# Optimization experiments

Hardware: AMD Instinct MI355X
Metric: run time of the kernel (lower is better)

Reference implementation:

```python
import jax, jax.numpy as jnp
import numpy as np

EPS = 1e-6
G, S, N, K, O = 3, 10, 5000, 20, 1000  # groups, subjects, particles, communities, otus


def setup_inputs() -> dict:
    key = jax.random.key(0)
    k1, k2, k3, k4, k5 = jax.random.split(key, 5)
    # particle count data (nonnegative reads per OTU)
    counts = jax.random.uniform(k1, (G, S, N, O), dtype=jnp.float32) * 10.0
    # community OTU distributions (rows on simplex)
    otu_dist = jax.nn.softmax(jax.random.normal(k2, (K, O), dtype=jnp.float32), axis=-1)
    # community assignment distribution per (group, subject), normalized over K
    comm_dist = jax.nn.softmax(jax.random.normal(k3, (K, G, S), dtype=jnp.float32), axis=0)
    # contamination weight per group in (0, 1)
    contam_weight = jax.nn.sigmoid(jax.random.normal(k4, (G,), dtype=jnp.float32)) * 0.1
    # contamination community OTU distribution per group
    contam_comm = jax.nn.softmax(jax.random.normal(k5, (G, O), dtype=jnp.float32), axis=-1)
    gamma = jnp.ones((), dtype=jnp.float32)
    return {
        'counts': counts,
        'otu_dist': otu_dist,
        'comm_dist': comm_dist,
        'contam_weight': contam_weight,
        'contam_comm': contam_comm,
        'gamma': gamma,
    }


def reference(counts, otu_dist, comm_dist, contam_weight, contam_comm, gamma):
    # contamination mixture per group: [G, K, O]
    cw = contam_weight[:, None, None]
    mix = otu_dist[None, :, :] * (1.0 - cw) + cw * contam_comm[:, None, :]
    log_mix = jnp.log(mix + EPS)
    # (counts[:, None, :] * log_mix[None]).sum(-1) over all (g, s) at once:
    # scores[g, s, n, k] = sum_o counts[g, s, n, o] * log_mix[g, k, o]
    scores = jnp.einsum('gsno,gko->gsnk', counts, log_mix)
    # + log(comm_dist[None, :, g, s]) broadcast over particles
    scores = scores + jnp.log(comm_dist + EPS).transpose(1, 2, 0)[:, :, None, :]
    # sparse_logsumexp over community axis (dim=1 in original per-subject matrix)
    x_star = jnp.max(scores, axis=-1, keepdims=True)
    lse = x_star[..., 0] + jnp.log(jnp.sum(jnp.exp(gamma * (scores - x_star)), axis=-1))
    return jnp.sum(lse)
```

## Files before the change

kernel.cpp:

```cpp
#include <hip/hip_runtime.h>


#define EPSF 1e-6f
constexpr int Gc = 3, Sc = 10, Nc = 5000, Kc = 20, Oc = 1000;
constexpr int ROWS_PER_G = Sc * Nc;
constexpr int GRAN_ROWS  = 8;
constexpr int GRANS_PER_G = ROWS_PER_G / GRAN_ROWS;
constexpr int LM_ELEMS = Kc * Oc;
constexpr int LM_ALLOC = LM_ELEMS + 32;

__device__ __forceinline__ float red32(float v) {
  v += __int_as_float(__builtin_amdgcn_update_dpp(0, __float_as_int(v), 0x111, 0xF, 0xF, true));
  v += __int_as_float(__builtin_amdgcn_update_dpp(0, __float_as_int(v), 0x112, 0xF, 0xF, true));
  v += __int_as_float(__builtin_amdgcn_update_dpp(0, __float_as_int(v), 0x114, 0xF, 0xF, true));
  v += __int_as_float(__builtin_amdgcn_update_dpp(0, __float_as_int(v), 0x118, 0xF, 0xF, true));
  v += __int_as_float(__builtin_amdgcn_update_dpp(0, __float_as_int(v), 0x142, 0xF, 0xF, true));
  return v;
}

__global__ __launch_bounds__(512, 2) void perturb_kernel(
    const float* __restrict__ counts, const float* __restrict__ otu,
    const float* __restrict__ comm,   const float* __restrict__ cw,
    const float* __restrict__ cc,     const float* __restrict__ gamma_p,
    float* __restrict__ out) {
  __shared__ float s_lm[LM_ALLOC];
  __shared__ float s_bias[Sc * Kc];

  const int tid  = threadIdx.x;
  const int bid  = blockIdx.x;
  const int g    = bid % Gc;
  const int bg   = bid / Gc;
  const int blocksg = (gridDim.x + (Gc - 1) - g) / Gc;

  const float cwg = cw[g];
  const float gam = gamma_p[0];

  for (int idx = tid; idx < LM_ALLOC; idx += blockDim.x) {
    float v = 0.f;
    if (idx < LM_ELEMS) {
      int o = idx % Oc;
      float mix = otu[idx] * (1.f - cwg) + cwg * cc[g * Oc + o];
      v = __logf(mix + EPSF);
    }
    s_lm[idx] = v;
  }
  for (int idx = tid; idx < Sc * Kc; idx += blockDim.x) {
    int s = idx / Kc, k = idx - s * Kc;
    s_bias[idx] = __logf(comm[(k * Gc + g) * Sc + s] + EPSF);
  }
  __syncthreads();

  const int wave = tid >> 6;
  const int lane = tid & 63;
  const int rl   = lane >> 5;
  const int osub = lane & 31;

  const int waveg  = bg * 8 + wave;
  const int nwaveg = blocksg * 8;

  float lsum = 0.f;

  for (int gr = waveg; gr < GRANS_PER_G; gr += nwaveg) {
    const int row0 = gr * GRAN_ROWS + rl * 4;
    const float* base = counts + (size_t)(g * ROWS_PER_G + row0) * Oc;

    float acc[4][Kc];
#pragma unroll
    for (int r = 0; r < 4; ++r)
#pragma unroll
      for (int k = 0; k < Kc; ++k) acc[r][k] = 0.f;

    for (int j = 0; j < 7; ++j) {
      const int ob = j * 128 + (osub << 2);
      float4 c0 = *(const float4*)(base + 0 * Oc + ob);
      float4 c1 = *(const float4*)(base + 1 * Oc + ob);
      float4 c2 = *(const float4*)(base + 2 * Oc + ob);
      float4 c3 = *(const float4*)(base + 3 * Oc + ob);
#pragma unroll
      for (int k = 0; k < Kc; ++k) {
        float4 L = *(const float4*)&s_lm[k * Oc + ob];
        acc[0][k] += c0.x * L.x + c0.y * L.y + c0.z * L.z + c0.w * L.w;
        acc[1][k] += c1.x * L.x + c1.y * L.y + c1.z * L.z + c1.w * L.w;
        acc[2][k] += c2.x * L.x + c2.y * L.y + c2.z * L.z + c2.w * L.w;
        acc[3][k] += c3.x * L.x + c3.y * L.y + c3.z * L.z + c3.w * L.w;
      }
    }
    {
      const int ob = 896 + (osub << 2);
      float4 c0 = {0,0,0,0}, c1 = {0,0,0,0}, c2 = {0,0,0,0}, c3 = {0,0,0,0};
      if (osub < 26) {
        c0 = *(const float4*)(base + 0 * Oc + ob);
        c1 = *(const float4*)(base + 1 * Oc + ob);
        c2 = *(const float4*)(base + 2 * Oc + ob);
        c3 = *(const float4*)(base + 3 * Oc + ob);
      }
#pragma unroll
      for (int k = 0; k < Kc; ++k) {
        float4 L = *(const float4*)&s_lm[k * Oc + ob];
        acc[0][k] += c0.x * L.x + c0.y * L.y + c0.z * L.z + c0.w * L.w;
        acc[1][k] += c1.x * L.x + c1.y * L.y + c1.z * L.z + c1.w * L.w;
        acc[2][k] += c2.x * L.x + c2.y * L.y + c2.z * L.z + c2.w * L.w;
        acc[3][k] += c3.x * L.x + c3.y * L.y + c3.z * L.z + c3.w * L.w;
      }
    }

#pragma unroll
    for (int r = 0; r < 4; ++r)
#pragma unroll
      for (int k = 0; k < Kc; ++k) acc[r][k] = red32(acc[r][k]);

    if ((lane & 31) == 31) {
#pragma unroll
      for (int r = 0; r < 4; ++r) {
        const int s = (row0 + r) / Nc;
        const float* bp = &s_bias[s * Kc];
        float m = -3.4e38f;
#pragma unroll
        for (int k = 0; k < Kc; ++k) {
          float x = acc[r][k] + bp[k];
          acc[r][k] = x;
          m = fmaxf(m, x);
        }
        float sum = 0.f;
#pragma unroll
        for (int k = 0; k < Kc; ++k) sum += __expf(gam * (acc[r][k] - m));
        lsum += m + __logf(sum);
      }
    }
  }

  if ((lane & 31) == 31) atomicAdd(out, lsum);
}

extern "C" void kernel_launch(void* const* d_in, const int* in_sizes, int n_in,
                              void* d_out, int out_size, void* d_ws, size_t ws_size,
                              hipStream_t stream) {
  const float* counts = (const float*)d_in[0];
  const float* otu    = (const float*)d_in[1];
  const float* comm   = (const float*)d_in[2];
  const float* cw     = (const float*)d_in[3];
  const float* cc     = (const float*)d_in[4];
  const float* gam    = (const float*)d_in[5];
  float* out = (float*)d_out;

  hipMemsetAsync(out, 0, sizeof(float), stream);
  hipLaunchKernelGGL(perturb_kernel, dim3(512), dim3(512), 0, stream,
                     counts, otu, comm, cw, cc, gam, out);
}
```

Before: 884.9 us.

## Split communities across half-waves and software-prefetch count tiles into registers

Each wave now handles 4 rows, and its two half-waves each compute 10 of the 20 communities instead of each taking different rows. The two partial log-sum-exp results are merged with a cross-half shuffle. Count tiles for the next column chunk and the next granule are loaded into registers before the current chunk is used, to hide global-load latency. This halves the accumulator registers per lane and overlaps loads with FMAs, but both half-waves now load the same count data, doubling vector-memory instructions per row.

```diff
diff --git a/kernel.cpp b/kernel.cpp
--- a/kernel.cpp
+++ b/kernel.cpp
@@ -4,8 +4,9 @@
 #define EPSF 1e-6f
 constexpr int Gc = 3, Sc = 10, Nc = 5000, Kc = 20, Oc = 1000;
 constexpr int ROWS_PER_G = Sc * Nc;
-constexpr int GRAN_ROWS  = 8;
+constexpr int GRAN_ROWS  = 4;
 constexpr int GRANS_PER_G = ROWS_PER_G / GRAN_ROWS;
+constexpr int KH = Kc / 2;
 constexpr int LM_ELEMS = Kc * Oc;
 constexpr int LM_ALLOC = LM_ELEMS + 32;
 
@@ -52,84 +53,110 @@
 
   const int wave = tid >> 6;
   const int lane = tid & 63;
-  const int rl   = lane >> 5;
+  const int kh   = lane >> 5;
+  const int k0   = kh * KH;
   const int osub = lane & 31;
+  const int ocol = osub << 2;
 
   const int waveg  = bg * 8 + wave;
   const int nwaveg = blocksg * 8;
 
   float lsum = 0.f;
 
-  for (int gr = waveg; gr < GRANS_PER_G; gr += nwaveg) {
-    const int row0 = gr * GRAN_ROWS + rl * 4;
-    const float* base = counts + (size_t)(g * ROWS_PER_G + row0) * Oc;
+  int gr = waveg;
+  float4 cur0, cur1, cur2, cur3;
+  const float* gbase = counts + (size_t)g * ROWS_PER_G * Oc;
 
-    float acc[4][Kc];
+  if (gr < GRANS_PER_G) {
+    const float* base = gbase + (size_t)gr * GRAN_ROWS * Oc + ocol;
+    cur0 = *(const float4*)(base + 0 * Oc);
+    cur1 = *(const float4*)(base + 1 * Oc);
+    cur2 = *(const float4*)(base + 2 * Oc);
+    cur3 = *(const float4*)(base + 3 * Oc);
+  }
+
+  for (; gr < GRANS_PER_G; gr += nwaveg) {
+    const int row0 = gr * GRAN_ROWS;
+    const float* base = gbase + (size_t)row0 * Oc + ocol;
+
+    float acc[GRAN_ROWS][KH];
 #pragma unroll
-    for (int r = 0; r < 4; ++r)
+    for (int r = 0; r < GRAN_ROWS; ++r)
 #pragma unroll
-      for (int k = 0; k < Kc; ++k) acc[r][k] = 0.f;
+      for (int k = 0; k < KH; ++k) acc[r][k] = 0.f;
 
+#pragma unroll
     for (int j = 0; j < 7; ++j) {
-      const int ob = j * 128 + (osub << 2);
-      float4 c0 = *(const float4*)(base + 0 * Oc + ob);
-      float4 c1 = *(const float4*)(base + 1 * Oc + ob);
-      float4 c2 = *(const float4*)(base + 2 * Oc + ob);
-      float4 c3 = *(const float4*)(base + 3 * Oc + ob);
+      float4 n0 = {0,0,0,0}, n1 = {0,0,0,0}, n2 = {0,0,0,0}, n3 = {0,0,0,0};
+      if (j < 6 || osub < 26) {
+        const float* nb = base + (j + 1) * 128;
+        n0 = *(const float4*)(nb + 0 * Oc);
+        n1 = *(const float4*)(nb + 1 * Oc);
+        n2 = *(const float4*)(nb + 2 * Oc);
+        n3 = *(const float4*)(nb + 3 * Oc);
+      }
+      const int ob = j * 128 + ocol;
 #pragma unroll
-      for (int k = 0; k < Kc; ++k) {
-        float4 L = *(const float4*)&s_lm[k * Oc + ob];
-        acc[0][k] += c0.x * L.x + c0.y * L.y + c0.z * L.z + c0.w * L.w;
-        acc[1][k] += c1.x * L.x + c1.y * L.y + c1.z * L.z + c1.w * L.w;
-        acc[2][k] += c2.x * L.x + c2.y * L.y + c2.z * L.z + c2.w * L.w;
-        acc[3][k] += c3.x * L.x + c3.y * L.y + c3.z * L.z + c3.w * L.w;
+      for (int k = 0; k < KH; ++k) {
+        float4 L = *(const float4*)&s_lm[(k0 + k) * Oc + ob];
+        acc[0][k] += cur0.x * L.x + cur0.y * L.y + cur0.z * L.z + cur0.w * L.w;
+        acc[1][k] += cur1.x * L.x + cur1.y * L.y + cur1.z * L.z + cur1.w * L.w;
+        acc[2][k] += cur2.x * L.x + cur2.y * L.y + cur2.z * L.z + cur2.w * L.w;
+        acc[3][k] += cur3.x * L.x + cur3.y * L.y + cur3.z * L.z + cur3.w * L.w;
       }
+      cur0 = n0; cur1 = n1; cur2 = n2; cur3 = n3;
     }
     {
-      const int ob = 896 + (osub << 2);
-      float4 c0 = {0,0,0,0}, c1 = {0,0,0,0}, c2 = {0,0,0,0}, c3 = {0,0,0,0};
-      if (osub < 26) {
-        c0 = *(const float4*)(base + 0 * Oc + ob);
-        c1 = *(const float4*)(base + 1 * Oc + ob);
-        c2 = *(const float4*)(base + 2 * Oc + ob);
-        c3 = *(const float4*)(base + 3 * Oc + ob);
-      }
+      const int ob = 896 + ocol;
 #pragma unroll
-      for (int k = 0; k < Kc; ++k) {
-        float4 L = *(const float4*)&s_lm[k * Oc + ob];
-        acc[0][k] += c0.x * L.x + c0.y * L.y + c0.z * L.z + c0.w * L.w;
-        acc[1][k] += c1.x * L.x + c1.y * L.y + c1.z * L.z + c1.w * L.w;
-        acc[2][k] += c2.x * L.x + c2.y * L.y + c2.z * L.z + c2.w * L.w;
-        acc[3][k] += c3.x * L.x + c3.y * L.y + c3.z * L.z + c3.w * L.w;
+      for (int k = 0; k < KH; ++k) {
+        float4 L = *(const float4*)&s_lm[(k0 + k) * Oc + ob];
+        acc[0][k] += cur0.x * L.x + cur0.y * L.y + cur0.z * L.z + cur0.w * L.w;
+        acc[1][k] += cur1.x * L.x + cur1.y * L.y + cur1.z * L.z + cur1.w * L.w;
+        acc[2][k] += cur2.x * L.x + cur2.y * L.y + cur2.z * L.z + cur2.w * L.w;
+        acc[3][k] += cur3.x * L.x + cur3.y * L.y + cur3.z * L.z + cur3.w * L.w;
       }
     }
 
+    const int grn = gr + nwaveg;
+    if (grn < GRANS_PER_G) {
+      const float* nb = gbase + (size_t)grn * GRAN_ROWS * Oc + ocol;
+      cur0 = *(const float4*)(nb + 0 * Oc);
+      cur1 = *(const float4*)(nb + 1 * Oc);
+      cur2 = *(const float4*)(nb + 2 * Oc);
+      cur3 = *(const float4*)(nb + 3 * Oc);
+    }
+
 #pragma unroll
-    for (int r = 0; r < 4; ++r)
+    for (int r = 0; r < GRAN_ROWS; ++r)
 #pragma unroll
-      for (int k = 0; k < Kc; ++k) acc[r][k] = red32(acc[r][k]);
+      for (int k = 0; k < KH; ++k) acc[r][k] = red32(acc[r][k]);
 
     if ((lane & 31) == 31) {
+      const int s = row0 / Nc;
+      const float* bp = &s_bias[s * Kc + k0];
 #pragma unroll
-      for (int r = 0; r < 4; ++r) {
-        const int s = (row0 + r) / Nc;
-        const float* bp = &s_bias[s * Kc];
-        float m = -3.4e38f;
+      for (int r = 0; r < GRAN_ROWS; ++r) {
+        float m_h = -3.4e38f;
 #pragma unroll
-        for (int k = 0; k < Kc; ++k) {
+        for (int k = 0; k < KH; ++k) {
           float x = acc[r][k] + bp[k];
           acc[r][k] = x;
-          m = fmaxf(m, x);
+          m_h = fmaxf(m_h, x);
         }
-        float sum = 0.f;
+        float s_h = 0.f;
 #pragma unroll
-        for (int k = 0; k < Kc; ++k) sum += __expf(gam * (acc[r][k] - m));
-        lsum += m + __logf(sum);
+        for (int k = 0; k < KH; ++k) s_h += __expf(gam * (acc[r][k] - m_h));
+        float m_o = __shfl_xor(m_h, 32);
+        float s_o = __shfl_xor(s_h, 32);
+        float m = fmaxf(m_h, m_o);
+        float ss = s_h * __expf(gam * (m_h - m)) + s_o * __expf(gam * (m_o - m));
+        if (lane == 31) lsum += m + __logf(ss);
       }
     }
   }
 
-  if ((lane & 31) == 31) atomicAdd(out, lsum);
+  if (lane == 31) atomicAdd(out, lsum);
 }
 
 extern "C" void kernel_launch(void* const* d_in, const int* in_sizes, int n_in,
```

Result: slower. 1.225 ms (+38.4%).
